# Performance work log

Hardware: AMD Instinct MI355X
Metric: run time of the kernel (lower is better)

## Reference

```python
import jax, jax.numpy as jnp
import numpy as np


def _chamfer(pred, target):
    # pred: (B, N, 3), target: (B, M, 3)
    # squared pairwise distances: ||p||^2 + ||t||^2 - 2 p.t
    p2 = jnp.sum(pred * pred, axis=-1)            # (B, N)
    t2 = jnp.sum(target * target, axis=-1)        # (B, M)
    cross = jnp.einsum('bnd,bmd->bnm', pred, target)  # (B, N, M)
    d = p2[:, :, None] + t2[:, None, :] - 2.0 * cross  # (B, N, M) squared dists
    dist1 = jnp.min(d, axis=2)  # (B, N) NN dist pred->target
    dist2 = jnp.min(d, axis=1)  # (B, M) NN dist target->pred
    return dist1, dist2


def setup_inputs() -> dict:
    key = jax.random.key(0)
    k1, k2 = jax.random.split(key)
    B, N, M = 4, 8192, 8192
    pred = jax.random.normal(k1, (B, N, 3), dtype=jnp.float32)
    target = jax.random.normal(k2, (B, M, 3), dtype=jnp.float32)
    return {"pred": pred, "target": target}


def reference(pred, target):
    dist1, dist2 = _chamfer(pred.astype(jnp.float32), target.astype(jnp.float32))
    loss = jnp.mean(dist1) + jnp.mean(dist2)
    return loss
```

## Files before the change

### kernel.cpp

```cpp
#include <hip/hip_runtime.h>


typedef short s8v __attribute__((ext_vector_type(8)));
typedef float f16v __attribute__((ext_vector_type(16)));

#define NPTS 8192
#define NB 4
#define CHUNKS 8

__device__ inline unsigned short f2bf(float f) {
    unsigned u = __builtin_bit_cast(unsigned, f);
    unsigned r = u + 0x7FFFu + ((u >> 16) & 1u);
    return (unsigned short)(r >> 16);
}
__device__ inline float bf2f(unsigned short s) {
    unsigned u = ((unsigned)s) << 16;
    return __builtin_bit_cast(float, u);
}
__device__ inline s8v i2s(int4 v) { return __builtin_bit_cast(s8v, v); }

__device__ inline f16v mfma_v0(s8v a, s8v b) {
    f16v d;
    asm volatile("v_mfma_f32_32x32x16_bf16 %0, %1, %2, 0"
                 : "=&v"(d) : "v"(a), "v"(b));
    return d;
}
__device__ inline float fmin3v(float a, float b, float c) {
    float d;
    asm volatile("v_min3_f32 %0, %1, %2, %3" : "=v"(d) : "v"(a), "v"(b), "v"(c));
    return d;
}
__device__ inline float mintree(const f16v& c, float mn) {
    float m0 = fmin3v(c[0],  c[1],  c[2]);
    float m1 = fmin3v(c[3],  c[4],  c[5]);
    float m2 = fmin3v(c[6],  c[7],  c[8]);
    float m3 = fmin3v(c[9],  c[10], c[11]);
    float m4 = fmin3v(c[12], c[13], c[14]);
    float m5 = fmin3v(m0, m1, m2);
    float m6 = fmin3v(m3, m4, c[15]);
    return fmin3v(m5, m6, mn);
}

__global__ __launch_bounds__(256) void chamfer_prep(
    const float* __restrict__ pred, const float* __restrict__ target,
    unsigned short* __restrict__ afmt, int* __restrict__ done)
{
    if (blockIdx.x == 0 && threadIdx.x == 0) *done = 0;

    const int g = blockIdx.x * 256 + threadIdx.x;
    const int c = g >> 15;
    const int rem = g & 32767;
    const float* src = (c == 0 ? pred : target) + (size_t)rem * 3;
    const float x = src[0], y = src[1], z = src[2];

    const unsigned short hx = f2bf(x), hy = f2bf(y), hz = f2bf(z);
    const float fx = bf2f(hx), fy = bf2f(hy), fz = bf2f(hz);
    const unsigned short lx = f2bf(x - fx), ly = f2bf(y - fy), lz = f2bf(z - fz);
    const float t2 = x*x + y*y + z*z;
    const unsigned short t2h = f2bf(t2);
    const unsigned short t2l = f2bf(t2 - bf2f(t2h));

    union { unsigned short u[16]; int4 v[2]; } A;
    A.u[0] = f2bf(-2.f*fx); A.u[1] = f2bf(-2.f*fy); A.u[2] = f2bf(-2.f*fz);
    A.u[3] = f2bf(-2.f*bf2f(lx)); A.u[4] = f2bf(-2.f*bf2f(ly)); A.u[5] = f2bf(-2.f*bf2f(lz));
    A.u[6] = A.u[0]; A.u[7] = A.u[1]; A.u[8] = A.u[2];
    A.u[9] = A.u[3]; A.u[10] = A.u[4]; A.u[11] = A.u[5];
    A.u[12] = t2h; A.u[13] = t2l; A.u[14] = 0; A.u[15] = 0;

    int4* ap = (int4*)(afmt + ((size_t)(1 - c) * 32768 + rem) * 16);
    ap[0] = A.v[0]; ap[1] = A.v[1];
}

__global__ __launch_bounds__(256) void chamfer_mfma(
    const float* __restrict__ pred, const float* __restrict__ target,
    const unsigned short* __restrict__ afmt,
    float* __restrict__ pmins)
{
    __shared__ int4 sbuf[2][512];

    const int dirb = blockIdx.y;
    const int dir  = dirb >> 2;
    const int b    = dirb & 3;
    const int chunk = blockIdx.z;
    const int tid  = threadIdx.x;
    const int wid  = tid >> 6;
    const int lane = tid & 63;
    const int half = lane >> 5;
    const int l31  = lane & 31;
    const int w    = blockIdx.x * 4 + wid;
    const int base = w * 128;

    const float* pc = ((dir == 0) ? pred : target) + (size_t)b * NPTS * 3;
    s8v bfrag[4];
#pragma unroll
    for (int q = 0; q < 4; ++q) {
        const float* sp = pc + (size_t)(base + q * 32 + l31) * 3;
        const float x = sp[0], y = sp[1], z = sp[2];
        const unsigned short hx = f2bf(x), hy = f2bf(y), hz = f2bf(z);
        const unsigned short lx = f2bf(x - bf2f(hx));
        const unsigned short ly = f2bf(y - bf2f(hy));
        const unsigned short lz = f2bf(z - bf2f(hz));
        union { unsigned short u[8]; s8v v; } F;
        if (half == 0) {
            F.u[0] = hx; F.u[1] = hy; F.u[2] = hz;
            F.u[3] = hx; F.u[4] = hy; F.u[5] = hz;
            F.u[6] = lx; F.u[7] = ly;
        } else {
            F.u[0] = lz; F.u[1] = lx; F.u[2] = ly; F.u[3] = lz;
            F.u[4] = 0x3F80; F.u[5] = 0x3F80; F.u[6] = 0; F.u[7] = 0;
        }
        bfrag[q] = F.v;
    }

    const size_t cbase = ((size_t)dir * NB + b) * NPTS;
    const int4* gsrc = (const int4*)(afmt + cbase * 16) + (size_t)chunk * 2048;

    float mn[4] = {1e30f, 1e30f, 1e30f, 1e30f};

    int4 g0 = gsrc[tid];
    int4 g1 = gsrc[256 + tid];

    for (int s = 0; s < 4; ++s) {
        const int cur = s & 1;
        __syncthreads();
        sbuf[cur][tid]       = g0;
        sbuf[cur][256 + tid] = g1;
        if (s < 3) {
            g0 = gsrc[(s + 1) * 512 + tid];
            g1 = gsrc[(s + 1) * 512 + 256 + tid];
        }
        __syncthreads();

        s8v Ac = i2s(sbuf[cur][l31 * 2 + half]);
#pragma unroll
        for (int t = 0; t < 8; ++t) {
            f16v c0 = mfma_v0(Ac, bfrag[0]);
            f16v c1 = mfma_v0(Ac, bfrag[1]);
            f16v c2 = mfma_v0(Ac, bfrag[2]);
            f16v c3 = mfma_v0(Ac, bfrag[3]);
            s8v An;
            if (t < 7) An = i2s(sbuf[cur][(t + 1) * 64 + l31 * 2 + half]);
            asm volatile("s_nop 7");
            mn[0] = mintree(c0, mn[0]);
            mn[1] = mintree(c1, mn[1]);
            mn[2] = mintree(c2, mn[2]);
            mn[3] = mintree(c3, mn[3]);
            Ac = An;
        }
    }

#pragma unroll
    for (int q = 0; q < 4; ++q) mn[q] = fminf(mn[q], __shfl_xor(mn[q], 32));

    if (half == 0) {
        float* dst = pmins + ((size_t)dirb * CHUNKS + chunk) * NPTS + base + l31;
        dst[0]  = mn[0];
        dst[32] = mn[1];
        dst[64] = mn[2];
        dst[96] = mn[3];
    }
}

__global__ __launch_bounds__(256) void chamfer_mergefin(
    const float* __restrict__ pred, const float* __restrict__ target,
    const float* __restrict__ pmins, float* __restrict__ partials,
    int* __restrict__ done, float* __restrict__ out)
{
    const int tid = threadIdx.x;
    const int t = blockIdx.x * 256 + tid;
    const int dirb = t >> 13;
    const int pr   = t & 8191;
    const int dir  = dirb >> 2;
    const int b    = dirb & 3;

    const float* mrow = pmins + (size_t)dirb * CHUNKS * NPTS + pr;
    float m = fminf(fminf(mrow[0*NPTS], mrow[1*NPTS]), mrow[2*NPTS]);
    m = fminf(fminf(m, mrow[3*NPTS]), mrow[4*NPTS]);
    m = fminf(fminf(m, mrow[5*NPTS]), mrow[6*NPTS]);
    m = fminf(m, mrow[7*NPTS]);

    const float* sp = ((dir == 0) ? pred : target) + ((size_t)b * NPTS + pr) * 3;
    const float p2 = sp[0]*sp[0] + sp[1]*sp[1] + sp[2]*sp[2];
    float v = (m + p2) * (1.0f / 32768.0f);

    __shared__ float s[256];
    __shared__ int lastFlag;
    s[tid] = v;
    __syncthreads();
    for (int wd = 128; wd > 0; wd >>= 1) {
        if (tid < wd) s[tid] += s[tid + wd];
        __syncthreads();
    }
    if (tid == 0) {
        __hip_atomic_store(&partials[blockIdx.x], s[0],
                           __ATOMIC_RELEASE, __HIP_MEMORY_SCOPE_AGENT);
        int prev = __hip_atomic_fetch_add(done, 1,
                           __ATOMIC_ACQ_REL, __HIP_MEMORY_SCOPE_AGENT);
        lastFlag = (prev == gridDim.x - 1);
    }
    __syncthreads();

    if (lastFlag) {
        float acc = __hip_atomic_load(&partials[tid],
                           __ATOMIC_ACQUIRE, __HIP_MEMORY_SCOPE_AGENT);
        s[tid] = acc;
        __syncthreads();
        for (int wd = 128; wd > 0; wd >>= 1) {
            if (tid < wd) s[tid] += s[tid + wd];
            __syncthreads();
        }
        if (tid == 0) out[0] = s[0];
    }
}

extern "C" void kernel_launch(void* const* d_in, const int* in_sizes, int n_in,
                              void* d_out, int out_size, void* d_ws, size_t ws_size,
                              hipStream_t stream)
{
    const float* pred   = (const float*)d_in[0];
    const float* target = (const float*)d_in[1];
    float* out = (float*)d_out;

    unsigned short* afmt = (unsigned short*)d_ws;
    float* pmins    = (float*)((char*)d_ws + (size_t)2 * 1024 * 1024);
    float* partials = (float*)((char*)d_ws + (size_t)4 * 1024 * 1024);
    int*   done     = (int*)((char*)d_ws + (size_t)5 * 1024 * 1024);

    chamfer_prep<<<256, 256, 0, stream>>>(pred, target, afmt, done);

    dim3 grid(16, 8, CHUNKS);
    chamfer_mfma<<<grid, 256, 0, stream>>>(pred, target, afmt, pmins);

    chamfer_mergefin<<<256, 256, 0, stream>>>(pred, target, pmins, partials, done, out);
}
```

Baseline: 37.03 us.

## Software-pipeline MFMA and min-reduction with double accumulators and permuted LDS layout

The inner loop is restructured so the four MFMAs for the next A tile are issued before the min-tree reduction of the previous tile's results, using two sets of accumulator registers (even and odd). This lets the VALU min3 work overlap matrix-core latency instead of waiting on an s_nop after each MFMA group. The LDS store index is also permuted so each lane reads a contiguous element (index n*64+lane) instead of the interleaved l31*2+half pattern. The cost is doubled accumulator register pressure (32 more VGPRs), which may lower occupancy.

```diff
diff --git a/kernel.cpp b/kernel.cpp
--- a/kernel.cpp
+++ b/kernel.cpp
@@ -117,37 +117,51 @@
 
     float mn[4] = {1e30f, 1e30f, 1e30f, 1e30f};
 
+    const int j = tid & 63;
+    const int wlo = (tid & 192) | ((j & 1) << 5) | (j >> 1);
+
     int4 g0 = gsrc[tid];
     int4 g1 = gsrc[256 + tid];
 
+#define LDT(n) i2s(sbuf[cur][(n)*64 + lane])
+#define MFMA4(r0,r1,r2,r3, Areg) \
+    r0 = mfma_v0(Areg, bfrag[0]); \
+    r1 = mfma_v0(Areg, bfrag[1]); \
+    r2 = mfma_v0(Areg, bfrag[2]); \
+    r3 = mfma_v0(Areg, bfrag[3]);
+#define MIN4(r0,r1,r2,r3) \
+    asm volatile("s_nop 7"); \
+    mn[0] = mintree(r0, mn[0]); \
+    mn[1] = mintree(r1, mn[1]); \
+    mn[2] = mintree(r2, mn[2]); \
+    mn[3] = mintree(r3, mn[3]);
+
     for (int s = 0; s < 4; ++s) {
         const int cur = s & 1;
         __syncthreads();
-        sbuf[cur][tid]       = g0;
-        sbuf[cur][256 + tid] = g1;
+        sbuf[cur][wlo]       = g0;
+        sbuf[cur][256 + wlo] = g1;
         if (s < 3) {
             g0 = gsrc[(s + 1) * 512 + tid];
             g1 = gsrc[(s + 1) * 512 + 256 + tid];
         }
         __syncthreads();
 
-        s8v Ac = i2s(sbuf[cur][l31 * 2 + half]);
-#pragma unroll
-        for (int t = 0; t < 8; ++t) {
-            f16v c0 = mfma_v0(Ac, bfrag[0]);
-            f16v c1 = mfma_v0(Ac, bfrag[1]);
-            f16v c2 = mfma_v0(Ac, bfrag[2]);
-            f16v c3 = mfma_v0(Ac, bfrag[3]);
-            s8v An;
-            if (t < 7) An = i2s(sbuf[cur][(t + 1) * 64 + l31 * 2 + half]);
-            asm volatile("s_nop 7");
-            mn[0] = mintree(c0, mn[0]);
-            mn[1] = mintree(c1, mn[1]);
-            mn[2] = mintree(c2, mn[2]);
-            mn[3] = mintree(c3, mn[3]);
-            Ac = An;
-        }
-    }
+        s8v Ae = LDT(0), Ao;
+        f16v e0, e1, e2, e3, o0, o1, o2, o3;
+        MFMA4(e0,e1,e2,e3, Ae)  Ao = LDT(1);
+        MFMA4(o0,o1,o2,o3, Ao)  Ae = LDT(2);  MIN4(e0,e1,e2,e3)
+        MFMA4(e0,e1,e2,e3, Ae)  Ao = LDT(3);  MIN4(o0,o1,o2,o3)
+        MFMA4(o0,o1,o2,o3, Ao)  Ae = LDT(4);  MIN4(e0,e1,e2,e3)
+        MFMA4(e0,e1,e2,e3, Ae)  Ao = LDT(5);  MIN4(o0,o1,o2,o3)
+        MFMA4(o0,o1,o2,o3, Ao)  Ae = LDT(6);  MIN4(e0,e1,e2,e3)
+        MFMA4(e0,e1,e2,e3, Ae)  Ao = LDT(7);  MIN4(o0,o1,o2,o3)
+        MFMA4(o0,o1,o2,o3, Ao)                MIN4(e0,e1,e2,e3)
+        MIN4(o0,o1,o2,o3)
+    }
+#undef LDT
+#undef MFMA4
+#undef MIN4
 
 #pragma unroll
     for (int q = 0; q < 4; ++q) mn[q] = fminf(mn[q], __shfl_xor(mn[q], 32));
```

New measurement: 38.72 us. +4.6%, slower.
